# Performance work log

Measured on AMD Instinct MI355X. Metric: run time of the kernel, lower is better.

The kernel has to match this reference:

```python
import jax, jax.numpy as jnp
import numpy as np

B, H, W, C = 16, 32, 32, 512
HEADS, DHEAD = 8, 64  # head * channel == C
GROUPS, EPS = 32, 1e-5


def setup_inputs() -> dict:
    key = jax.random.key(0)
    ks = jax.random.split(key, 6)
    return {
        "x": jax.random.normal(ks[0], (B, H, W, C), jnp.float32),
        "gn_gamma": jnp.ones((C,), jnp.float32),
        "gn_beta": jnp.zeros((C,), jnp.float32),
        "wq": jax.random.normal(ks[1], (C, HEADS * DHEAD), jnp.float32) * 0.02,
        "wk": jax.random.normal(ks[2], (C, HEADS * DHEAD), jnp.float32) * 0.02,
        "wv": jax.random.normal(ks[3], (C, HEADS * DHEAD), jnp.float32) * 0.02,
        "conv_w": jax.random.normal(ks[4], (3, 3, HEADS * DHEAD, C), jnp.float32) * 0.02,
        "conv_b": jnp.zeros((C,), jnp.float32),
    }


def _group_norm(x, gamma, beta):
    b, h, w, c = x.shape
    xg = x.reshape(b, h, w, GROUPS, c // GROUPS)
    mean = jnp.mean(xg, axis=(1, 2, 4), keepdims=True)
    var = jnp.var(xg, axis=(1, 2, 4), keepdims=True)
    xn = (xg - mean) * jax.lax.rsqrt(var + EPS)
    return xn.reshape(b, h, w, c) * gamma + beta


def reference(x, gn_gamma, gn_beta, wq, wk, wv, conv_w, conv_b):
    xn = _group_norm(x, gn_gamma, gn_beta)          # [B,H,W,C]
    t = xn.reshape(B, H * W, C)                      # tokens [B,S,C]
    q = (t @ wq).reshape(B, H * W, HEADS, DHEAD)
    k = (t @ wk).reshape(B, H * W, HEADS, DHEAD)
    v = (t @ wv).reshape(B, H * W, HEADS, DHEAD)
    scale = 1.0 / jnp.sqrt(jnp.asarray(DHEAD, q.dtype))
    scores = jnp.einsum("bqhd,bkhd->bhqk", q, k) * scale  # [B,HEADS,S,S]
    weights = jax.nn.softmax(scores, axis=-1)
    out = jnp.einsum("bhqk,bkhd->bqhd", weights, v)       # [B,S,HEADS,DHEAD]
    out = out.reshape(B, H, W, HEADS * DHEAD)
    y = jax.lax.conv_general_dilated(
        out, conv_w, window_strides=(1, 1), padding=((1, 1), (1, 1)),
        dimension_numbers=("NHWC", "HWIO", "NHWC")) + conv_b
    return y + x
```

## Files before the change

kernel.cpp:

```cpp
#include <hip/hip_runtime.h>
#include <hip/hip_bf16.h>

#define Bn 16
#define Cc 512
#define Ss 1024
#define HEADS 8
#define DHEAD 64
#define GROUPS 32
#define CPG 16
#define EPSv 1e-5f
#define Mtok (Bn*Ss)
#define QKVS 1536
#define PROW 34
#define PIMG (PROW*PROW)

typedef __hip_bfloat16 bf16;
typedef __attribute__((ext_vector_type(8))) short short8;
typedef __attribute__((ext_vector_type(4))) float f32x4;

union U4 { uint4 u; bf16 h[8]; };
union B4 { ushort4 u; bf16 h[4]; };

__device__ __forceinline__ void stage16(const bf16* g, bf16* l) {
    __builtin_amdgcn_global_load_lds((const __attribute__((address_space(1))) void*)g,
                                     (__attribute__((address_space(3))) void*)l,
                                     16, 0, 0);
}

__global__ __launch_bounds__(256) void wtrans(const float* __restrict__ src,
                                              bf16* __restrict__ dst) {
    size_t off = (size_t)blockIdx.y * 262144;
    int t = blockIdx.x * 256 + threadIdx.x;
    int n = t & 511, k8 = (t >> 9) * 8;
    const float* s = src + off + (size_t)k8 * 512 + n;
    U4 o;
#pragma unroll
    for (int j = 0; j < 8; j++) o.h[j] = __float2bfloat16(s[(size_t)j * 512]);
    *(uint4*)(dst + off + (size_t)n * 512 + k8) = o.u;
}

__global__ __launch_bounds__(256) void gn_stats(const float* __restrict__ x,
                                                float* __restrict__ stats) {
    int bg = blockIdx.x;
    int b = bg >> 5, g = bg & 31;
    int tid = threadIdx.x;
    const size_t base = (size_t)b * Ss * Cc + g * CPG;
    float sum = 0.f, sq = 0.f;
    for (int i = tid; i < 4096; i += 256) {
        int s = i >> 2, c4 = (i & 3) * 4;
        float4 t = *(const float4*)(x + base + (size_t)s * Cc + c4);
        sum += t.x + t.y + t.z + t.w;
        sq  += t.x * t.x + t.y * t.y + t.z * t.z + t.w * t.w;
    }
    __shared__ float s1[4], s2[4];
#pragma unroll
    for (int off = 32; off > 0; off >>= 1) {
        sum += __shfl_down(sum, off);
        sq  += __shfl_down(sq,  off);
    }
    if ((tid & 63) == 0) { s1[tid >> 6] = sum; s2[tid >> 6] = sq; }
    __syncthreads();
    if (tid == 0) {
        float S = s1[0] + s1[1] + s1[2] + s1[3];
        float Q = s2[0] + s2[1] + s2[2] + s2[3];
        float mean = S * (1.f / 16384.f);
        float var  = Q * (1.f / 16384.f) - mean * mean;
        stats[bg * 2 + 0] = mean;
        stats[bg * 2 + 1] = rsqrtf(var + EPSv);
    }
}

__global__ __launch_bounds__(256) void gn_apply(const float* __restrict__ x,
                                                const float* __restrict__ stats,
                                                const float* __restrict__ gamma,
                                                const float* __restrict__ beta,
                                                bf16* __restrict__ xn) {
    size_t i = (size_t)blockIdx.x * 256 + threadIdx.x;
    size_t e = i * 4;
    int c0 = (int)(e & (Cc - 1));
    int token = (int)(e >> 9);
    int b = token >> 10;
    int g = c0 >> 4;
    float mean = stats[(b * 32 + g) * 2 + 0];
    float rstd = stats[(b * 32 + g) * 2 + 1];
    float4 t  = *(const float4*)(x + e);
    float4 gm = *(const float4*)(gamma + c0);
    float4 bt = *(const float4*)(beta + c0);
    B4 o;
    o.h[0] = __float2bfloat16((t.x - mean) * rstd * gm.x + bt.x);
    o.h[1] = __float2bfloat16((t.y - mean) * rstd * gm.y + bt.y);
    o.h[2] = __float2bfloat16((t.z - mean) * rstd * gm.z + bt.z);
    o.h[3] = __float2bfloat16((t.w - mean) * rstd * gm.w + bt.w);
    *(ushort4*)(xn + e) = o.u;
}

__global__ __launch_bounds__(256) void zero_pad(bf16* __restrict__ Pad) {
    int idx = blockIdx.x * 256 + threadIdx.x;
    int b = idx / (132 * 64);
    int rem = idx - b * 132 * 64;
    int t = rem >> 6, seg = rem & 63;
    int r, c;
    if (t < 34)      { r = 0;  c = t; }
    else if (t < 68) { r = 33; c = t - 34; }
    else { int u = t - 68; r = 1 + (u >> 1); c = (u & 1) * 33; }
    uint4 z = {0u, 0u, 0u, 0u};
    *(uint4*)(Pad + ((size_t)b * PIMG + r * PROW + c) * Cc + seg * 8) = z;
}

__global__ __launch_bounds__(256) void gemm_qkv(const bf16* __restrict__ A,
                                                const bf16* __restrict__ Wt,
                                                bf16* __restrict__ C) {
    __shared__ __align__(16) bf16 As[128][32];
    __shared__ __align__(16) bf16 Bs[128][32];
    int tid = threadIdx.x;
    int wave = tid >> 6, lane = tid & 63;
    int l15 = lane & 15, quad = lane >> 4;
    int wm = wave >> 1, wn = wave & 1;
    int m0 = blockIdx.y * 128, n0 = blockIdx.x * 128;
    int lr = lane >> 2, kseg = (lane & 3) * 8;
    int ar0 = wave * 32 + lr;

    const bf16* ga = A  + (size_t)(m0 + ar0) * Cc + kseg;
    const bf16* gb = Wt + (size_t)(n0 + ar0) * Cc + kseg;
    bf16* la0 = &As[wave * 32][0];
    bf16* la1 = &As[wave * 32 + 16][0];
    bf16* lb0 = &Bs[wave * 32][0];
    bf16* lb1 = &Bs[wave * 32 + 16][0];

    f32x4 acc[4][4] = {};
    for (int k0 = 0; k0 < 512; k0 += 32) {
        __syncthreads();
        stage16(ga + k0,                  la0);
        stage16(ga + k0 + (size_t)16 * Cc, la1);
        stage16(gb + k0,                  lb0);
        stage16(gb + k0 + (size_t)16 * Cc, lb1);
        __syncthreads();
        short8 af[4], bfv[4];
#pragma unroll
        for (int mt = 0; mt < 4; mt++) af[mt]  = *(const short8*)&As[wm * 64 + mt * 16 + l15][quad * 8];
#pragma unroll
        for (int nt = 0; nt < 4; nt++) bfv[nt] = *(const short8*)&Bs[wn * 64 + nt * 16 + l15][quad * 8];
#pragma unroll
        for (int mt = 0; mt < 4; mt++)
#pragma unroll
            for (int nt = 0; nt < 4; nt++)
                acc[mt][nt] = __builtin_amdgcn_mfma_f32_16x16x32_bf16(af[mt], bfv[nt], acc[mt][nt], 0, 0, 0);
    }
#pragma unroll
    for (int mt = 0; mt < 4; mt++)
#pragma unroll
        for (int r = 0; r < 4; r++) {
            size_t row = (size_t)(m0 + wm * 64 + mt * 16 + quad * 4 + r) * QKVS + n0 + wn * 64 + l15;
#pragma unroll
            for (int nt = 0; nt < 4; nt++)
                C[row + nt * 16] = __float2bfloat16(acc[mt][nt][r]);
        }
}

__global__ __launch_bounds__(256) void attention_mfma(const bf16* __restrict__ QKV,
                                                      bf16* __restrict__ Pad) {
    int blk = blockIdx.x;
    int qt = blk & 15;
    int bh = blk >> 4;
    int h = bh & (HEADS - 1), b = bh >> 3;
    int tid = threadIdx.x;
    int wave = tid >> 6, lane = tid & 63;
    int l15 = lane & 15, quad = lane >> 4;

    __shared__ __align__(16) bf16 Ks[2][32][72];
    __shared__ __align__(16) bf16 Vt[2][64][40];
    __shared__ __align__(16) bf16 Ps[4][16][40];

    const size_t base = (size_t)b * Ss * QKVS + h * DHEAD;
    const bf16* kbase = QKV + base + 512;
    const bf16* vbase = QKV + base + 1024;

    int q0 = qt * 64 + wave * 16;
    const bf16* qrow = QKV + base + (size_t)(q0 + l15) * QKVS + quad * 8;
    short8 qf0 = *(const short8*)(qrow);
    short8 qf1 = *(const short8*)(qrow + 32);

    f32x4 oacc[4] = {{0.f,0.f,0.f,0.f},{0.f,0.f,0.f,0.f},{0.f,0.f,0.f,0.f},{0.f,0.f,0.f,0.f}};
    float lsum[4] = {0.f, 0.f, 0.f, 0.f};
    const f32x4 zero4 = {0.f, 0.f, 0.f, 0.f};

    int tok = tid & 31, d0 = (tid >> 5) * 8;

    uint4 nk, nv;
    {
        const size_t rb = (size_t)tok * QKVS + d0;
        nk = *(const uint4*)(kbase + rb);
        nv = *(const uint4*)(vbase + rb);
    }
    *(uint4*)&Ks[0][tok][d0] = nk;
    { U4 u; u.u = nv;
#pragma unroll
      for (int i = 0; i < 8; i++) Vt[0][d0 + i][tok] = u.h[i]; }
    __syncthreads();

    for (int c = 0; c < 32; ++c) {
        int buf = c & 1;
        if (c + 1 < 32) {
            const size_t rb = (size_t)((c + 1) * 32 + tok) * QKVS + d0;
            nk = *(const uint4*)(kbase + rb);
            nv = *(const uint4*)(vbase + rb);
        }
#pragma unroll
        for (int kg = 0; kg < 2; kg++) {
            short8 kf0 = *(const short8*)&Ks[buf][kg * 16 + l15][quad * 8];
            short8 kf1 = *(const short8*)&Ks[buf][kg * 16 + l15][32 + quad * 8];
            f32x4 s = __builtin_amdgcn_mfma_f32_16x16x32_bf16(qf0, kf0, zero4, 0, 0, 0);
            s = __builtin_amdgcn_mfma_f32_16x16x32_bf16(qf1, kf1, s, 0, 0, 0);
#pragma unroll
            for (int r = 0; r < 4; r++) {
                float p = __expf(s[r] * 0.125f);
                lsum[r] += p;
                Ps[wave][quad * 4 + r][kg * 16 + l15] = __float2bfloat16(p);
            }
        }
        short8 pf = *(const short8*)&Ps[wave][l15][quad * 8];
#pragma unroll
        for (int dt = 0; dt < 4; dt++) {
            short8 vf = *(const short8*)&Vt[buf][dt * 16 + l15][quad * 8];
            oacc[dt] = __builtin_amdgcn_mfma_f32_16x16x32_bf16(pf, vf, oacc[dt], 0, 0, 0);
        }
        if (c + 1 < 32) {
            *(uint4*)&Ks[buf ^ 1][tok][d0] = nk;
            U4 u; u.u = nv;
#pragma unroll
            for (int i = 0; i < 8; i++) Vt[buf ^ 1][d0 + i][tok] = u.h[i];
        }
        __syncthreads();
    }

#pragma unroll
    for (int r = 0; r < 4; r++) {
#pragma unroll
        for (int m = 1; m < 16; m <<= 1) lsum[r] += __shfl_xor(lsum[r], m);
    }
#pragma unroll
    for (int r = 0; r < 4; r++) {
        float inv = 1.f / lsum[r];
        int s = q0 + quad * 4 + r;
        size_t rowoff = ((size_t)(b * PROW + (s >> 5) + 1) * PROW + (s & 31) + 1) * Cc + h * DHEAD;
#pragma unroll
        for (int dt = 0; dt < 4; dt++)
            Pad[rowoff + dt * 16 + l15] = __float2bfloat16(oacc[dt][r] * inv);
    }
}

__global__ __launch_bounds__(256, 2) void conv_mfma(const bf16* __restrict__ Pad,
                                                    const bf16* __restrict__ Wct,
                                                    const float* __restrict__ bias,
                                                    const float* __restrict__ xres,
                                                    float* __restrict__ out) {
    __shared__ __align__(16) bf16 As[2][136 * 32];
    __shared__ __align__(16) bf16 Bs[2][3][128][32];

    int tid = threadIdx.x;
    int wave = tid >> 6, lane = tid & 63;
    int l15 = lane & 15, quad = lane >> 4;
    int wm = wave >> 1, wn = wave & 1;
    int m0 = blockIdx.y * 128, n0 = blockIdx.x * 128;
    int b = m0 >> 10, oh0 = (m0 & 1023) >> 5;

    int lr = lane >> 2, kseg = (lane & 3) * 8;
    const bf16* gwp = Wct + (size_t)(n0 + wave * 32 + lr) * Cc + kseg;

    int t1 = tid >> 2,          r1 = t1 / 34, col1 = t1 - r1 * 34;
    int t2 = (tid + 256) >> 2,  r2 = t2 / 34, col2 = t2 - r2 * 34;
    int t3 = (tid + 512) >> 2,  r3 = t3 / 34, col3 = t3 - r3 * 34;
    int ks = (tid & 3) * 8;
    const size_t dyStride = (size_t)PROW * Cc;
    const bf16* pA1 = Pad + ((size_t)b * PIMG + (size_t)(oh0 + r1) * PROW + col1) * Cc + ks;
    const bf16* pA2 = Pad + ((size_t)b * PIMG + (size_t)(oh0 + r2) * PROW + col2) * Cc + ks;
    const bf16* pA3 = Pad + ((size_t)b * PIMG + (size_t)(oh0 + r3) * PROW + col3) * Cc + ks;

    int arow[4];
#pragma unroll
    for (int mt = 0; mt < 4; mt++)
        arow[mt] = (wm * 2 + (mt >> 1)) * 34 + (mt & 1) * 16 + l15;

    auto stage_it = [&](int it, int p) {
        int dyi = it >> 4;
        int k0 = (it & 15) << 5;
        size_t aoff = (size_t)dyi * dyStride + k0;
        stage16(pA1 + aoff, &As[p][wave * 512]);
        stage16(pA2 + aoff, &As[p][2048 + wave * 512]);
        if (tid < 32) stage16(pA3 + aoff, &As[p][4096]);
        const bf16* gW = gwp + (size_t)(dyi * 3) * (Cc * Cc) + k0;
#pragma unroll
        for (int t = 0; t < 3; t++) {
            const bf16* gwt = gW + (size_t)t * (Cc * Cc);
            stage16(gwt,                   &Bs[p][t][wave * 32][0]);
            stage16(gwt + (size_t)16 * Cc, &Bs[p][t][wave * 32 + 16][0]);
        }
    };

    f32x4 acc[4][4] = {};
    stage_it(0, 0);
    for (int it = 0; it < 48; ++it) {
        int p = it & 1;
        if (it + 1 < 48) {
            stage_it(it + 1, p ^ 1);
            asm volatile("s_waitcnt vmcnt(8)" ::: "memory");
        } else {
            asm volatile("s_waitcnt vmcnt(0)" ::: "memory");
        }
        __builtin_amdgcn_s_barrier();

        short8 af[3][4], bfv[3][4];
#pragma unroll
        for (int dxi = 0; dxi < 3; dxi++) {
#pragma unroll
            for (int mt = 0; mt < 4; mt++)
                af[dxi][mt] = *(const short8*)&As[p][(arow[mt] + dxi) * 32 + quad * 8];
#pragma unroll
            for (int nt = 0; nt < 4; nt++)
                bfv[dxi][nt] = *(const short8*)&Bs[p][dxi][wn * 64 + nt * 16 + l15][quad * 8];
        }
        asm volatile("s_waitcnt lgkmcnt(0)" ::: "memory");
        __builtin_amdgcn_sched_barrier(0);
        __builtin_amdgcn_s_barrier();

#pragma unroll
        for (int dxi = 0; dxi < 3; dxi++)
#pragma unroll
            for (int mt = 0; mt < 4; mt++)
#pragma unroll
                for (int nt = 0; nt < 4; nt++)
                    acc[mt][nt] = __builtin_amdgcn_mfma_f32_16x16x32_bf16(af[dxi][mt], bfv[dxi][nt], acc[mt][nt], 0, 0, 0);
    }

#pragma unroll
    for (int mt = 0; mt < 4; mt++)
#pragma unroll
        for (int r = 0; r < 4; r++) {
            size_t row = (size_t)(m0 + wm * 64 + mt * 16 + quad * 4 + r) * Cc + n0 + wn * 64 + l15;
#pragma unroll
            for (int nt = 0; nt < 4; nt++) {
                int n = n0 + wn * 64 + nt * 16 + l15;
                out[row + nt * 16] = acc[mt][nt][r] + bias[n] + xres[row + nt * 16];
            }
        }
}

extern "C" void kernel_launch(void* const* d_in, const int* in_sizes, int n_in,
                              void* d_out, int out_size, void* d_ws, size_t ws_size,
                              hipStream_t stream) {
    const float* x     = (const float*)d_in[0];
    const float* gamma = (const float*)d_in[1];
    const float* beta  = (const float*)d_in[2];
    const float* wq    = (const float*)d_in[3];
    const float* wk    = (const float*)d_in[4];
    const float* wv    = (const float*)d_in[5];
    const float* convw = (const float*)d_in[6];
    const float* convb = (const float*)d_in[7];
    float* out = (float*)d_out;

    char* ws = (char*)d_ws;
    bf16*  pad   = (bf16*)ws;
    float* stats = (float*)ws;
    bf16*  xn    = (bf16*)(ws + 4096);
    bf16*  wt    = (bf16*)(ws + 4096 + ((size_t)16 << 20));
    bf16*  qkv   = (bf16*)(ws + ((size_t)19 << 20));
    bf16*  wct   = (bf16*)(ws + ((size_t)67 << 20));

    wtrans<<<dim3(128, 1), 256, 0, stream>>>(wq, wt);
    wtrans<<<dim3(128, 1), 256, 0, stream>>>(wk, wt + 262144);
    wtrans<<<dim3(128, 1), 256, 0, stream>>>(wv, wt + 524288);
    wtrans<<<dim3(128, 9), 256, 0, stream>>>(convw, wct);

    gn_stats<<<dim3(Bn * GROUPS), 256, 0, stream>>>(x, stats);
    gn_apply<<<dim3(Mtok * Cc / (4 * 256)), 256, 0, stream>>>(x, stats, gamma, beta, xn);

    gemm_qkv<<<dim3(QKVS / 128, Mtok / 128), 256, 0, stream>>>(xn, wt, qkv);

    zero_pad<<<dim3(528), 256, 0, stream>>>(pad);
    attention_mfma<<<dim3(Bn * HEADS * (Ss / 64)), 256, 0, stream>>>(qkv, pad);

    conv_mfma<<<dim3(Cc / 128, Mtok / 128), 256, 0, stream>>>(pad, wct, convb, x, out);
}
```

Before: 321.5 us.

## Compute transposed attention scores and pass P via shuffles instead of LDS

The attention kernel now computes S^T and O^T by swapping the MFMA operands, so each lane holds the probabilities for a single query. The P operand for the PV MFMA is assembled in registers with packed bf16 cross-lane shuffles, which removes the per-wave LDS round trip for P. The row sum drops from four 16-lane reductions to one two-step reduction, and the final output is written as 4-wide vector stores. The cost is eight shuffles per chunk and extra register packing.

Measured after the change: 326.2 us. Within noise of the previous version (+1.5%).

```diff
diff --git a/kernel.cpp b/kernel.cpp
--- a/kernel.cpp
+++ b/kernel.cpp
@@ -25,6 +25,12 @@
     __builtin_amdgcn_global_load_lds((const __attribute__((address_space(1))) void*)g,
                                      (__attribute__((address_space(3))) void*)l,
                                      16, 0, 0);
+}
+
+__device__ __forceinline__ unsigned int pkbf(float a, float b) {
+    union { __hip_bfloat16 h; unsigned short u; } ua, ub;
+    ua.h = __float2bfloat16(a); ub.h = __float2bfloat16(b);
+    return ((unsigned int)ub.u << 16) | ua.u;
 }
 
 __global__ __launch_bounds__(256) void wtrans(const float* __restrict__ src,
@@ -169,7 +175,6 @@
 
     __shared__ __align__(16) bf16 Ks[2][32][72];
     __shared__ __align__(16) bf16 Vt[2][64][40];
-    __shared__ __align__(16) bf16 Ps[4][16][40];
 
     const size_t base = (size_t)b * Ss * QKVS + h * DHEAD;
     const bf16* kbase = QKV + base + 512;
@@ -180,11 +185,14 @@
     short8 qf0 = *(const short8*)(qrow);
     short8 qf1 = *(const short8*)(qrow + 32);
 
-    f32x4 oacc[4] = {{0.f,0.f,0.f,0.f},{0.f,0.f,0.f,0.f},{0.f,0.f,0.f,0.f},{0.f,0.f,0.f,0.f}};
-    float lsum[4] = {0.f, 0.f, 0.f, 0.f};
+    f32x4 oaccT[4] = {{0.f,0.f,0.f,0.f},{0.f,0.f,0.f,0.f},{0.f,0.f,0.f,0.f},{0.f,0.f,0.f,0.f}};
+    float lsum = 0.f;
     const f32x4 zero4 = {0.f, 0.f, 0.f, 0.f};
 
     int tok = tid & 31, d0 = (tid >> 5) * 8;
+
+    int srcA = (((quad * 2) & 3) * 16 + l15);
+    int srcB = (((quad * 2 + 1) & 3) * 16 + l15);
 
     uint4 nk, nv;
     {
@@ -205,24 +213,39 @@
             nk = *(const uint4*)(kbase + rb);
             nv = *(const uint4*)(vbase + rb);
         }
-#pragma unroll
-        for (int kg = 0; kg < 2; kg++) {
-            short8 kf0 = *(const short8*)&Ks[buf][kg * 16 + l15][quad * 8];
-            short8 kf1 = *(const short8*)&Ks[buf][kg * 16 + l15][32 + quad * 8];
-            f32x4 s = __builtin_amdgcn_mfma_f32_16x16x32_bf16(qf0, kf0, zero4, 0, 0, 0);
-            s = __builtin_amdgcn_mfma_f32_16x16x32_bf16(qf1, kf1, s, 0, 0, 0);
-#pragma unroll
-            for (int r = 0; r < 4; r++) {
-                float p = __expf(s[r] * 0.125f);
-                lsum[r] += p;
-                Ps[wave][quad * 4 + r][kg * 16 + l15] = __float2bfloat16(p);
-            }
-        }
-        short8 pf = *(const short8*)&Ps[wave][l15][quad * 8];
+        unsigned int pk[2][2];
+#pragma unroll
+        for (int kb = 0; kb < 2; kb++) {
+            short8 kf0 = *(const short8*)&Ks[buf][kb * 16 + l15][quad * 8];
+            short8 kf1 = *(const short8*)&Ks[buf][kb * 16 + l15][32 + quad * 8];
+            f32x4 s = __builtin_amdgcn_mfma_f32_16x16x32_bf16(kf0, qf0, zero4, 0, 0, 0);
+            s = __builtin_amdgcn_mfma_f32_16x16x32_bf16(kf1, qf1, s, 0, 0, 0);
+            float p0 = __expf(s[0] * 0.125f);
+            float p1 = __expf(s[1] * 0.125f);
+            float p2 = __expf(s[2] * 0.125f);
+            float p3 = __expf(s[3] * 0.125f);
+            lsum += (p0 + p1) + (p2 + p3);
+            pk[kb][0] = pkbf(p0, p1);
+            pk[kb][1] = pkbf(p2, p3);
+        }
+        unsigned int a0 = __shfl((int)pk[0][0], srcA);
+        unsigned int a1 = __shfl((int)pk[0][1], srcA);
+        unsigned int a2 = __shfl((int)pk[1][0], srcA);
+        unsigned int a3 = __shfl((int)pk[1][1], srcA);
+        unsigned int b0 = __shfl((int)pk[0][0], srcB);
+        unsigned int b1 = __shfl((int)pk[0][1], srcB);
+        unsigned int b2 = __shfl((int)pk[1][0], srcB);
+        unsigned int b3 = __shfl((int)pk[1][1], srcB);
+        union { short8 s8; unsigned int u[4]; } PT;
+        bool lo = (quad < 2);
+        PT.u[0] = lo ? a0 : a2;
+        PT.u[1] = lo ? a1 : a3;
+        PT.u[2] = lo ? b0 : b2;
+        PT.u[3] = lo ? b1 : b3;
 #pragma unroll
         for (int dt = 0; dt < 4; dt++) {
             short8 vf = *(const short8*)&Vt[buf][dt * 16 + l15][quad * 8];
-            oacc[dt] = __builtin_amdgcn_mfma_f32_16x16x32_bf16(pf, vf, oacc[dt], 0, 0, 0);
+            oaccT[dt] = __builtin_amdgcn_mfma_f32_16x16x32_bf16(vf, PT.s8, oaccT[dt], 0, 0, 0);
         }
         if (c + 1 < 32) {
             *(uint4*)&Ks[buf ^ 1][tok][d0] = nk;
@@ -233,19 +256,18 @@
         __syncthreads();
     }
 
-#pragma unroll
-    for (int r = 0; r < 4; r++) {
-#pragma unroll
-        for (int m = 1; m < 16; m <<= 1) lsum[r] += __shfl_xor(lsum[r], m);
-    }
-#pragma unroll
-    for (int r = 0; r < 4; r++) {
-        float inv = 1.f / lsum[r];
-        int s = q0 + quad * 4 + r;
-        size_t rowoff = ((size_t)(b * PROW + (s >> 5) + 1) * PROW + (s & 31) + 1) * Cc + h * DHEAD;
-#pragma unroll
-        for (int dt = 0; dt < 4; dt++)
-            Pad[rowoff + dt * 16 + l15] = __float2bfloat16(oacc[dt][r] * inv);
+    lsum += __shfl_xor(lsum, 16);
+    lsum += __shfl_xor(lsum, 32);
+    float inv = 1.f / lsum;
+
+    int s = q0 + l15;
+    size_t rowoff = ((size_t)(b * PROW + (s >> 5) + 1) * PROW + (s & 31) + 1) * Cc + h * DHEAD;
+#pragma unroll
+    for (int dt = 0; dt < 4; dt++) {
+        B4 o;
+#pragma unroll
+        for (int r = 0; r < 4; r++) o.h[r] = __float2bfloat16(oaccT[dt][r] * inv);
+        *(ushort4*)(Pad + rowoff + dt * 16 + quad * 4) = o.u;
     }
 }
 
```
